# Kernel optimization log

Measured on AMD Instinct MI355X. Metric: run time of the kernel, lower is better.

The kernel has to match this reference:

```python
import jax, jax.numpy as jnp
import numpy as np

HEADS = 8


def setup_inputs() -> dict:
    key = jax.random.key(0)
    ks = jax.random.split(key, 9)
    B, C, H, W = 16, 512, 32, 32
    d = C // HEADS
    scale = d ** -0.5
    return {
        "x": jax.random.normal(ks[0], (B, C, H, W), dtype=jnp.float32),
        "Wq": jax.random.normal(ks[1], (C, C), dtype=jnp.float32) * (C ** -0.5),
        "bq": jax.random.normal(ks[2], (C,), dtype=jnp.float32) * 0.02,
        "Wk": jax.random.normal(ks[3], (C, C), dtype=jnp.float32) * (C ** -0.5),
        "bk": jax.random.normal(ks[4], (C,), dtype=jnp.float32) * 0.02,
        "Wv": jax.random.normal(ks[5], (C, C), dtype=jnp.float32) * (C ** -0.5),
        "bv": jax.random.normal(ks[6], (C,), dtype=jnp.float32) * 0.02,
        "rel_h": jax.random.normal(ks[7], (d, H, 1), dtype=jnp.float32) * scale,
        "rel_w": jax.random.normal(ks[8], (d, 1, W), dtype=jnp.float32) * scale,
    }


def reference(x, Wq, bq, Wk, bk, Wv, bv, rel_h, rel_w):
    B, C, H, W = x.shape
    heads = HEADS
    d = C // heads
    scale = d ** -0.5
    N = H * W
    xf = x.reshape(B, C, N)  # 1x1 conv == per-pixel linear over channels
    q = (jnp.einsum('oc,bcn->bon', Wq, xf) + bq[:, None]).reshape(B, heads, d, N)
    k = (jnp.einsum('oc,bcn->bon', Wk, xf) + bk[:, None]).reshape(B, heads, d, N)
    v = (jnp.einsum('oc,bcn->bon', Wv, xf) + bv[:, None]).reshape(B, heads, d, N)
    q = q * scale
    # content-content scores [B, heads, N, N]
    cc = jnp.einsum('bhdi,bhdj->bhij', q, k)
    # relative position bias table [d, N], projected by q
    cp_tab = (rel_h + rel_w).reshape(d, N)
    cp = jnp.einsum('bhdi,dj->bhij', q, cp_tab)
    beta = jax.nn.softmax(cc + cp, axis=-1)
    attn = jnp.einsum('bhij,bhdj->bhid', beta, v)  # [B, heads, N, d]
    # original does .view(x.shape) on [b,h,i,d] -> keep same raw reshape
    return attn.reshape(B, C, H, W)
```

## Files before the change

### kernel.cpp

```cpp
#include <hip/hip_runtime.h>
#include <hip/hip_bf16.h>
#include <stdint.h>

typedef unsigned short u16;
typedef u16 u16x8 __attribute__((ext_vector_type(8)));
typedef u16 u16x4 __attribute__((ext_vector_type(4)));
typedef unsigned int u32x4 __attribute__((ext_vector_type(4)));
typedef __bf16 bf16x8 __attribute__((ext_vector_type(8)));
typedef float f32x4 __attribute__((ext_vector_type(4)));

#define MFMA16(a, b, c) __builtin_amdgcn_mfma_f32_16x16x32_bf16((a), (b), (c), 0, 0, 0)

#define SCALE_Q 0.18033688011112042f

__device__ __forceinline__ u16 f2b(float f) {
    union { float f; unsigned u; } v; v.f = f;
    unsigned r = v.u + 0x7FFFu + ((v.u >> 16) & 1u);
    return (u16)(r >> 16);
}
__device__ __forceinline__ u16 f2b_h(float f) {
    union { float f; unsigned u; } v; v.f = f;
    return (u16)((v.u + 0x8000u) >> 16);
}
__device__ __forceinline__ unsigned pk2(float lo, float hi) {
    unsigned r;
    asm("v_cvt_pk_bf16_f32 %0, %1, %2" : "=v"(r) : "v"(lo), "v"(hi));
    return r;
}

__device__ __forceinline__ void gload16(const u16* g, u16* l) {
    __builtin_amdgcn_global_load_lds(
        (const __attribute__((address_space(1))) unsigned int*)g,
        (__attribute__((address_space(3))) unsigned int*)l, 16, 0, 0);
}

__global__ __launch_bounds__(256) void prep(
    const float* __restrict__ x,
    const float* __restrict__ Wq, const float* __restrict__ Wk,
    const float* __restrict__ Wv,
    u16* __restrict__ wb, u16* __restrict__ xT) {
    __shared__ __align__(16) u16 Ls[128 * 72];
    const int tid = threadIdx.x;

    if (blockIdx.x < 384) {
        int g = blockIdx.x * 256 + tid;
        int which = g >> 15;
        const float* src = which == 0 ? Wq : (which == 1 ? Wk : Wv);
        int off = (g & 32767) * 8;
        f32x4 a = *(const f32x4*)(src + off);
        f32x4 b = *(const f32x4*)(src + off + 4);
        u16x8 o;
#pragma unroll
        for (int i = 0; i < 4; ++i) { o[i] = f2b_h(a[i]); o[4 + i] = f2b_h(b[i]); }
        *(u16x8*)(wb + (size_t)g * 8) = o;
        return;
    }

    const int bid = blockIdx.x - 384;
    const int b  = bid >> 6;
    const int ct = (bid >> 3) & 7;
    const int nt = bid & 7;
    const int C0 = ct * 64, N0 = nt * 128;
    const float* xb = x + ((size_t)b << 19);

#pragma unroll
    for (int rep = 0; rep < 4; ++rep) {
        int id = tid + rep * 256;
        int oct = id >> 7, n = id & 127;
        const float* xp = xb + (size_t)(C0 + oct * 8) * 1024 + N0 + n;
        u16x8 xv;
#pragma unroll
        for (int k = 0; k < 8; ++k) xv[k] = f2b_h(xp[k * 1024]);
        *(u16x8*)(Ls + n * 72 + oct * 8) = xv;
    }
    __syncthreads();
#pragma unroll
    for (int rep = 0; rep < 4; ++rep) {
        int id = tid + rep * 256;
        int n = id >> 3, c8 = id & 7;
        *(u16x8*)(xT + ((size_t)b << 19) + (size_t)(N0 + n) * 512 + C0 + c8 * 8) =
            *(u16x8*)(Ls + n * 72 + c8 * 8);
    }
}

__global__ __launch_bounds__(256, 4) void qkv_proj(
    const u16* __restrict__ xT, const u16* __restrict__ wb,
    const float* __restrict__ bq, const float* __restrict__ bk,
    const float* __restrict__ bv,
    const float* __restrict__ rel_h, const float* __restrict__ rel_w,
    u16* __restrict__ qws, u16* __restrict__ kws, u16* __restrict__ vws) {
    __shared__ __align__(16) u16 Xs2[2][128 * 32];
    __shared__ __align__(16) u16 Ws2[2][128 * 32];

    const int tid  = threadIdx.x;
    const int wave = tid >> 6, lane = tid & 63;
    const int quad = lane >> 4, l16 = lane & 15;
    const int wr = wave >> 1, wc = wave & 1;

    const int id = blockIdx.x;
    const int nt = id & 7;
    const int r  = id >> 3;
    const int o0 = r & 3;
    const int r2 = r >> 2;
    const int mm = r2 % 3;
    const int b  = r2 / 3;
    const int N0 = nt * 128;
    const int O0 = o0 * 128;

    const u16*   W    = wb + (size_t)mm * 262144;
    const float* bias = mm == 0 ? bq : (mm == 1 ? bk : bv);
    const u16*   Xb   = xT + ((size_t)b << 19);

    const int srow = wave * 16 + (lane >> 2);
    const int sl   = ((lane & 3) ^ (lane >> 4)) * 8;
    const u16* Xg = Xb + (size_t)(N0 + srow) * 512 + sl;
    const u16* Wg = W  + (size_t)(O0 + srow) * 512 + sl;
    u16* const XL = &Xs2[0][0];
    u16* const WL = &Ws2[0][0];
    const int wofs = wave * 512;

    auto STAGE = [&](int kt, int buf) {
        gload16(Xg + kt * 32,         XL + buf * 4096 + wofs);
        gload16(Xg + kt * 32 + 32768, XL + buf * 4096 + 2048 + wofs);
        gload16(Wg + kt * 32,         WL + buf * 4096 + wofs);
        gload16(Wg + kt * 32 + 32768, WL + buf * 4096 + 2048 + wofs);
    };

    f32x4 acc[4][4] = {};
    const int fsl = (quad ^ (l16 >> 2)) * 8;

    STAGE(0, 0);

    auto step = [&](int kt, int cur) {
        __syncthreads();
        if (kt < 15) STAGE(kt + 1, cur ^ 1);
        const u16* Xc = XL + cur * 4096;
        const u16* Wc = WL + cur * 4096;
        bf16x8 af[4], bfr[4];
#pragma unroll
        for (int mi = 0; mi < 4; ++mi)
            af[mi] = *(const bf16x8*)(Xc + (wr * 64 + mi * 16 + l16) * 32 + fsl);
#pragma unroll
        for (int ni = 0; ni < 4; ++ni)
            bfr[ni] = *(const bf16x8*)(Wc + (wc * 64 + ni * 16 + l16) * 32 + fsl);
        __builtin_amdgcn_s_setprio(1);
#pragma unroll
        for (int mi = 0; mi < 4; ++mi)
#pragma unroll
            for (int ni = 0; ni < 4; ++ni)
                acc[mi][ni] = MFMA16(af[mi], bfr[ni], acc[mi][ni]);
        __builtin_amdgcn_s_setprio(0);
    };

    for (int k2 = 0; k2 < 8; ++k2) {
        step(2 * k2,     0);
        step(2 * k2 + 1, 1);
    }

#pragma unroll
    for (int mi = 0; mi < 4; ++mi) {
#pragma unroll
        for (int ni = 0; ni < 4; ++ni) {
            int o  = O0 + wc * 64 + ni * 16 + l16;
            int h  = o >> 6, dd = o & 63;
            size_t bh = (size_t)b * 8 + h;
            float bv_ = bias[o];
            int n0 = N0 + wr * 64 + mi * 16 + quad * 4;
            if (mm == 2) {
                u16x4 pk;
#pragma unroll
                for (int rr = 0; rr < 4; ++rr) pk[rr] = f2b(acc[mi][ni][rr] + bv_);
                int qq = (n0 >> 2) & 3, ss = (n0 >> 4) & 1;
                int np = (n0 & ~31) | (qq * 8 + ss * 4);
                int slot = ((np >> 3) & 7) ^ (dd & 7);
                int np2 = (np & ~63) | (slot << 3) | (np & 7);
                *(u16x4*)(vws + (bh * 64 + dd) * 1024 + np2) = pk;
            } else if (mm == 0) {
#pragma unroll
                for (int rr = 0; rr < 4; ++rr)
                    qws[(bh * 1024 + (n0 + rr)) * 64 + dd] =
                        f2b((acc[mi][ni][rr] + bv_) * SCALE_Q);
            } else {
                float th = rel_h[dd * 32 + (n0 >> 5)];
                f32x4 tw = *(const f32x4*)(rel_w + dd * 32 + (n0 & 31));
#pragma unroll
                for (int rr = 0; rr < 4; ++rr) {
                    int n = n0 + rr;
                    int sdd = (((dd >> 3) ^ (n & 7)) << 3) | (dd & 7);
                    kws[(bh * 1024 + n) * 64 + sdd] =
                        f2b(acc[mi][ni][rr] + bv_ + th + tw[rr]);
                }
            }
        }
    }
}

__global__ __launch_bounds__(512, 4) void attn(
    const u16* __restrict__ qws, const u16* __restrict__ kws,
    const u16* __restrict__ vws, float* __restrict__ out) {
    __shared__ __align__(16) u16 KPb[2][64 * 64];
    __shared__ __align__(16) u16 Vtb[2][64 * 64];

    const int tid  = threadIdx.x;
    const int wave = tid >> 6, lane = tid & 63;
    const int quad = lane >> 4, l16 = lane & 15;
    const int id = blockIdx.x;
    const int h  = id & 7;
    const int qt = (id >> 3) & 3;
    const int b  = id >> 5;
    const size_t bh = (size_t)b * 8 + h;

    const u16* Q = qws + (bh * 1024 + (size_t)qt * 256) * 64;
    const u16* K = kws + bh * 65536;
    const u16* V = vws + bh * 65536;

    const int lrow = wave * 8 + (lane >> 3);
    const int lc8  = lane & 7;
    const u16* Kl = K + (size_t)lrow * 64 + lc8 * 8;
    const u16* Vl = V + ((size_t)lrow << 10) + lc8 * 8;
    u16* const KP0 = &KPb[0][0];
    u16* const Vt0 = &Vtb[0][0];
    const int wofs = wave * 512;

    bf16x8 qf[2][2];
#pragma unroll
    for (int ni = 0; ni < 2; ++ni)
#pragma unroll
        for (int ks = 0; ks < 2; ++ks)
            qf[ni][ks] = *(const bf16x8*)(Q + (wave * 32 + ni * 16 + l16) * 64 + ks * 32 + quad * 8);

    const int xsw = (l16 & 7) << 4;
    const int xk0 = (quad * 16) ^ xsw;
    const int xk1 = (64 + quad * 16) ^ xsw;

    f32x4 accO[4][2] = {};
    f32x4 s4[2] = {};

    gload16(Kl, KP0 + wofs);
    gload16(Vl, Vt0 + wofs);

    auto body = [&](int jt, int cur) {
        __syncthreads();
        if (jt < 15) {
            int nxt = cur ^ 1;
            gload16(Kl + (jt + 1) * 4096, KP0 + nxt * 4096 + wofs);
            gload16(Vl + (jt + 1) * 64,  Vt0 + nxt * 4096 + wofs);
        }
        const char* KP = (const char*)(KP0 + cur * 4096);
        const char* Vt = (const char*)(Vt0 + cur * 4096);

        f32x4 aST[4][2] = {};
#pragma unroll
        for (int ks = 0; ks < 2; ++ks) {
            const int xo = ks ? xk1 : xk0;
            bf16x8 kf[4];
#pragma unroll
            for (int mj = 0; mj < 4; ++mj)
                kf[mj] = *(const bf16x8*)(KP + (mj * 16 + l16) * 128 + xo);
            __builtin_amdgcn_s_setprio(1);
#pragma unroll
            for (int mj = 0; mj < 4; ++mj)
#pragma unroll
                for (int ni = 0; ni < 2; ++ni)
                    aST[mj][ni] = MFMA16(kf[mj], qf[ni][ks], aST[mj][ni]);
            __builtin_amdgcn_s_setprio(0);
        }

#pragma unroll
        for (int mj = 0; mj < 4; ++mj)
#pragma unroll
            for (int ni = 0; ni < 2; ++ni) {
                f32x4 p;
#pragma unroll
                for (int rr = 0; rr < 4; ++rr)
                    p[rr] = __builtin_amdgcn_exp2f(aST[mj][ni][rr]);
                s4[ni] += p;
                aST[mj][ni] = p;
            }

#pragma unroll
        for (int ks2 = 0; ks2 < 2; ++ks2) {
            union { u32x4 u; bf16x8 b; } pfr[2];
#pragma unroll
            for (int ni = 0; ni < 2; ++ni) {
                pfr[ni].u[0] = pk2(aST[2 * ks2][ni][0],     aST[2 * ks2][ni][1]);
                pfr[ni].u[1] = pk2(aST[2 * ks2][ni][2],     aST[2 * ks2][ni][3]);
                pfr[ni].u[2] = pk2(aST[2 * ks2 + 1][ni][0], aST[2 * ks2 + 1][ni][1]);
                pfr[ni].u[3] = pk2(aST[2 * ks2 + 1][ni][2], aST[2 * ks2 + 1][ni][3]);
            }
            const int xo = ks2 ? xk1 : xk0;
            bf16x8 vf[4];
#pragma unroll
            for (int md = 0; md < 4; ++md)
                vf[md] = *(const bf16x8*)(Vt + (md * 16 + l16) * 128 + xo);
            __builtin_amdgcn_s_setprio(1);
#pragma unroll
            for (int md = 0; md < 4; ++md)
#pragma unroll
                for (int ni = 0; ni < 2; ++ni)
                    accO[md][ni] = MFMA16(vf[md], pfr[ni].b, accO[md][ni]);
            __builtin_amdgcn_s_setprio(0);
        }
    };

    for (int j2 = 0; j2 < 8; ++j2) {
        body(2 * j2,     0);
        body(2 * j2 + 1, 1);
    }

#pragma unroll
    for (int ni = 0; ni < 2; ++ni) {
        float rs = (s4[ni][0] + s4[ni][1]) + (s4[ni][2] + s4[ni][3]);
        rs += __shfl_xor(rs, 16);
        rs += __shfl_xor(rs, 32);
        float inv = 1.0f / rs;
        int i = qt * 256 + wave * 32 + ni * 16 + l16;
#pragma unroll
        for (int md = 0; md < 4; ++md) {
            f32x4 pk;
#pragma unroll
            for (int rr = 0; rr < 4; ++rr) pk[rr] = accO[md][ni][rr] * inv;
            *(f32x4*)(out + (bh * 1024 + i) * 64 + md * 16 + quad * 4) = pk;
        }
    }
}

extern "C" void kernel_launch(void* const* d_in, const int* in_sizes, int n_in,
                              void* d_out, int out_size, void* d_ws, size_t ws_size,
                              hipStream_t stream) {
    const float* x  = (const float*)d_in[0];
    const float* Wq = (const float*)d_in[1];
    const float* bq = (const float*)d_in[2];
    const float* Wk = (const float*)d_in[3];
    const float* bk = (const float*)d_in[4];
    const float* Wv = (const float*)d_in[5];
    const float* bv = (const float*)d_in[6];
    const float* rh = (const float*)d_in[7];
    const float* rw = (const float*)d_in[8];
    float* out = (float*)d_out;

    u16* kws = (u16*)d_ws;
    u16* vws = kws + 8388608;
    u16* qws = vws + 8388608;
    u16* wb  = qws + 8388608;
    u16* xT  = (u16*)d_out;

    prep<<<1408, 256, 0, stream>>>(x, Wq, Wk, Wv, wb, xT);
    qkv_proj<<<1536, 256, 0, stream>>>(xT, wb, bq, bk, bv, rh, rw, qws, kws, vws);
    attn<<<512, 512, 0, stream>>>(qws, kws, vws, out);
}
```

Measured before the change: 184.7 us.

## Enlarge QKV projection tile to 256x128 with 512 threads and register-staged prefetch

The QKV projection kernel now uses 512-thread blocks, each covering 256 pixels by 128 output channels with a 64-wide K step. This halves the block count and improves reuse of the weight tile. The direct-to-LDS double-buffered async loads are replaced by register-prefetched global loads stored into a single padded LDS buffer (row stride 72), with two barriers per step. The larger tile lowers global traffic per FLOP, but having only one LDS buffer and the extra barrier may reduce overlap, and the added registers may limit occupancy.

Result: slower. 242.0 us (+31.0%).

```diff
diff --git a/kernel.cpp b/kernel.cpp
--- a/kernel.cpp
+++ b/kernel.cpp
@@ -83,14 +83,14 @@
     }
 }
 
-__global__ __launch_bounds__(256, 4) void qkv_proj(
+__global__ __launch_bounds__(512, 4) void qkv_proj(
     const u16* __restrict__ xT, const u16* __restrict__ wb,
     const float* __restrict__ bq, const float* __restrict__ bk,
     const float* __restrict__ bv,
     const float* __restrict__ rel_h, const float* __restrict__ rel_w,
     u16* __restrict__ qws, u16* __restrict__ kws, u16* __restrict__ vws) {
-    __shared__ __align__(16) u16 Xs2[2][128 * 32];
-    __shared__ __align__(16) u16 Ws2[2][128 * 32];
+    __shared__ __align__(16) u16 Xs[256 * 72];
+    __shared__ __align__(16) u16 Ws[128 * 72];
 
     const int tid  = threadIdx.x;
     const int wave = tid >> 6, lane = tid & 63;
@@ -98,63 +98,65 @@
     const int wr = wave >> 1, wc = wave & 1;
 
     const int id = blockIdx.x;
-    const int nt = id & 7;
-    const int r  = id >> 3;
-    const int o0 = r & 3;
-    const int r2 = r >> 2;
+    const int nt = id & 3;
+    const int o0 = (id >> 2) & 3;
+    const int r2 = id >> 4;
     const int mm = r2 % 3;
     const int b  = r2 / 3;
-    const int N0 = nt * 128;
+    const int N0 = nt * 256;
     const int O0 = o0 * 128;
 
     const u16*   W    = wb + (size_t)mm * 262144;
     const float* bias = mm == 0 ? bq : (mm == 1 ? bk : bv);
     const u16*   Xb   = xT + ((size_t)b << 19);
 
-    const int srow = wave * 16 + (lane >> 2);
-    const int sl   = ((lane & 3) ^ (lane >> 4)) * 8;
-    const u16* Xg = Xb + (size_t)(N0 + srow) * 512 + sl;
-    const u16* Wg = W  + (size_t)(O0 + srow) * 512 + sl;
-    u16* const XL = &Xs2[0][0];
-    u16* const WL = &Ws2[0][0];
-    const int wofs = wave * 512;
-
-    auto STAGE = [&](int kt, int buf) {
-        gload16(Xg + kt * 32,         XL + buf * 4096 + wofs);
-        gload16(Xg + kt * 32 + 32768, XL + buf * 4096 + 2048 + wofs);
-        gload16(Wg + kt * 32,         WL + buf * 4096 + wofs);
-        gload16(Wg + kt * 32 + 32768, WL + buf * 4096 + 2048 + wofs);
-    };
+    const int sr = tid >> 3, sc8 = tid & 7;
+
+    u16x8 xr[4], wrg[2];
+#pragma unroll
+    for (int rp = 0; rp < 4; ++rp)
+        xr[rp]  = *(const u16x8*)(Xb + (size_t)(N0 + sr + rp * 64) * 512 + sc8 * 8);
+#pragma unroll
+    for (int rp = 0; rp < 2; ++rp)
+        wrg[rp] = *(const u16x8*)(W  + (size_t)(O0 + sr + rp * 64) * 512 + sc8 * 8);
 
     f32x4 acc[4][4] = {};
-    const int fsl = (quad ^ (l16 >> 2)) * 8;
-
-    STAGE(0, 0);
-
-    auto step = [&](int kt, int cur) {
+
+    for (int kt = 0; kt < 8; ++kt) {
         __syncthreads();
-        if (kt < 15) STAGE(kt + 1, cur ^ 1);
-        const u16* Xc = XL + cur * 4096;
-        const u16* Wc = WL + cur * 4096;
-        bf16x8 af[4], bfr[4];
-#pragma unroll
-        for (int mi = 0; mi < 4; ++mi)
-            af[mi] = *(const bf16x8*)(Xc + (wr * 64 + mi * 16 + l16) * 32 + fsl);
-#pragma unroll
-        for (int ni = 0; ni < 4; ++ni)
-            bfr[ni] = *(const bf16x8*)(Wc + (wc * 64 + ni * 16 + l16) * 32 + fsl);
-        __builtin_amdgcn_s_setprio(1);
-#pragma unroll
-        for (int mi = 0; mi < 4; ++mi)
+#pragma unroll
+        for (int rp = 0; rp < 4; ++rp)
+            *(u16x8*)(Xs + (sr + rp * 64) * 72 + sc8 * 8) = xr[rp];
+#pragma unroll
+        for (int rp = 0; rp < 2; ++rp)
+            *(u16x8*)(Ws + (sr + rp * 64) * 72 + sc8 * 8) = wrg[rp];
+        __syncthreads();
+        if (kt < 7) {
+            int c0 = (kt + 1) * 64;
+#pragma unroll
+            for (int rp = 0; rp < 4; ++rp)
+                xr[rp]  = *(const u16x8*)(Xb + (size_t)(N0 + sr + rp * 64) * 512 + c0 + sc8 * 8);
+#pragma unroll
+            for (int rp = 0; rp < 2; ++rp)
+                wrg[rp] = *(const u16x8*)(W  + (size_t)(O0 + sr + rp * 64) * 512 + c0 + sc8 * 8);
+        }
+#pragma unroll
+        for (int kk = 0; kk < 2; ++kk) {
+            bf16x8 af[4], bfr[4];
+#pragma unroll
+            for (int mi = 0; mi < 4; ++mi)
+                af[mi] = *(bf16x8*)(Xs + (wr * 64 + mi * 16 + l16) * 72 + kk * 32 + quad * 8);
 #pragma unroll
             for (int ni = 0; ni < 4; ++ni)
-                acc[mi][ni] = MFMA16(af[mi], bfr[ni], acc[mi][ni]);
-        __builtin_amdgcn_s_setprio(0);
-    };
-
-    for (int k2 = 0; k2 < 8; ++k2) {
-        step(2 * k2,     0);
-        step(2 * k2 + 1, 1);
+                bfr[ni] = *(bf16x8*)(Ws + (wc * 64 + ni * 16 + l16) * 72 + kk * 32 + quad * 8);
+            __builtin_amdgcn_s_setprio(1);
+#pragma unroll
+            for (int mi = 0; mi < 4; ++mi)
+#pragma unroll
+                for (int ni = 0; ni < 4; ++ni)
+                    acc[mi][ni] = MFMA16(af[mi], bfr[ni], acc[mi][ni]);
+            __builtin_amdgcn_s_setprio(0);
+        }
     }
 
 #pragma unroll
@@ -346,6 +348,6 @@
     u16* xT  = (u16*)d_out;
 
     prep<<<1408, 256, 0, stream>>>(x, Wq, Wk, Wv, wb, xT);
-    qkv_proj<<<1536, 256, 0, stream>>>(xT, wb, bq, bk, bv, rh, rw, qws, kws, vws);
+    qkv_proj<<<768, 512, 0, stream>>>(xT, wb, bq, bk, bv, rh, rw, qws, kws, vws);
     attn<<<512, 512, 0, stream>>>(qws, kws, vws, out);
 }
```
